# Kernel optimization log

Measured on AMD Instinct MI355X. Metric: run time of the kernel, lower is better.

Reference implementation:

```python
import jax, jax.numpy as jnp
import numpy as np

N = 20000
E = 500000
NS = 128
NT = 128
BN_EPS = 1e-3
DIMS = [NS, 2 * NT, 4 * NT, 2 * NT, NT, NT]


def setup_inputs() -> dict:
    key = jax.random.key(0)
    ks = jax.random.split(key, 32)
    inp = {
        "x": jax.random.normal(ks[0], (N, NS), jnp.float32),
        "edge_index": jax.random.randint(ks[1], (2, E), 0, N),
        "edge_attr": jax.random.uniform(ks[2], (E,), jnp.float32),
    }
    for i in range(5):
        din, dout = DIMS[i], DIMS[i + 1]
        inp[f"W{i+1}"] = jax.random.normal(ks[3 + i], (din, dout), jnp.float32) * (1.0 / np.sqrt(din)).astype(np.float32)
        inp[f"b{i+1}"] = jnp.zeros((dout,), jnp.float32)
    for i in range(4):
        d = DIMS[i + 1]
        inp[f"g{i+1}"] = 1.0 + 0.1 * jax.random.normal(ks[10 + i], (d,), jnp.float32)
        inp[f"be{i+1}"] = 0.1 * jax.random.normal(ks[14 + i], (d,), jnp.float32)
        inp[f"m{i+1}"] = 0.1 * jax.random.normal(ks[18 + i], (d,), jnp.float32)
        inp[f"v{i+1}"] = jax.random.uniform(ks[22 + i], (d,), jnp.float32, minval=0.5, maxval=1.5)
    return inp


def gcn_norm(edge_index, edge_attr, n):
    # PyG gcn_norm with self-loops (fill value 1) and symmetric degree norm.
    loop = jnp.arange(n)
    row = jnp.concatenate([edge_index[0], loop])
    col = jnp.concatenate([edge_index[1], loop])
    w = jnp.concatenate([edge_attr, jnp.ones((n,), edge_attr.dtype)])
    deg = jax.ops.segment_sum(w, col, num_segments=n)
    dinv = jnp.where(deg > 0, jax.lax.rsqrt(deg), 0.0)
    return row, col, dinv[row] * w * dinv[col]


def gcn_conv(h, W, b, row, col, norm, n):
    # out[col] += norm * (h @ W)[row]; then add bias (PyG GCNConv).
    hw = h @ W
    agg = jax.ops.segment_sum(hw[row] * norm[:, None], col, num_segments=n)
    return agg + b


def bn_eval(h, g, be, m, v):
    return (h - m) * jax.lax.rsqrt(v + BN_EPS) * g + be


def reference(x, edge_index, edge_attr,
              W1, b1, W2, b2, W3, b3, W4, b4, W5, b5,
              g1, be1, m1, v1, g2, be2, m2, v2,
              g3, be3, m3, v3, g4, be4, m4, v4):
    n = x.shape[0]
    row, col, norm = gcn_norm(edge_index, edge_attr, n)  # cached=True: shared by all layers
    h = jax.nn.sigmoid(bn_eval(gcn_conv(x, W1, b1, row, col, norm, n), g1, be1, m1, v1))
    h = jax.nn.sigmoid(bn_eval(gcn_conv(h, W2, b2, row, col, norm, n), g2, be2, m2, v2))
    h = jax.nn.sigmoid(bn_eval(gcn_conv(h, W3, b3, row, col, norm, n), g3, be3, m3, v3))
    h = jax.nn.sigmoid(bn_eval(gcn_conv(h, W4, b4, row, col, norm, n), g4, be4, m4, v4))
    h = jax.nn.sigmoid(gcn_conv(h, W5, b5, row, col, norm, n))
    # dropout is identity in eval mode
    x11 = h.T @ h  # [NT, NT]
    x12 = 0.5 * (x11 + x11.T)
    return x12 - jnp.diag(jnp.diag(x12))
```

## Files before the change

### kernel.cpp

```cpp
#include <hip/hip_runtime.h>
#include <hip/hip_bf16.h>
#include <hip/hip_fp8.h>
#include <cstdint>
#include <cstddef>
#include <cstring>

typedef __hip_bfloat16 bf16;
typedef unsigned char fp8;
typedef __attribute__((ext_vector_type(8))) short short8;
typedef __attribute__((ext_vector_type(4))) float f32x4;
typedef __attribute__((ext_vector_type(2))) float f32x2;

#define NSF 128
#define BN_EPS 1e-3f
#define NR 4
#define SCK 2048


__global__ void passA_kernel(const int* __restrict__ ei, int* __restrict__ fill,
                             int* __restrict__ loc, int E, int n, int rsize) {
    int idx = blockIdx.x * blockDim.x + threadIdx.x;
    if (idx < E) {
        int r = ei[idx];
        int c = ei[E + idx];
        int slot = c * NR + r / rsize;
        loc[idx] = atomicAdd(&fill[slot], 1);
    } else if (idx < E + n) {
        int i = idx - E;
        int slot = i * NR + i / rsize;
        loc[idx] = atomicAdd(&fill[slot], 1);
    }
}


__global__ void scan1_kernel(const int* __restrict__ cnt, int* __restrict__ blksum, int total) {
    __shared__ int red[256];
    int base = blockIdx.x * SCK + threadIdx.x * 8;
    int s = 0;
    #pragma unroll
    for (int i = 0; i < 8; ++i) {
        int idx = base + i;
        if (idx < total) s += cnt[idx];
    }
    red[threadIdx.x] = s;
    __syncthreads();
    for (int off2 = 128; off2 > 0; off2 >>= 1) {
        if (threadIdx.x < off2) red[threadIdx.x] += red[threadIdx.x + off2];
        __syncthreads();
    }
    if (threadIdx.x == 0) blksum[blockIdx.x] = red[0];
}

__global__ void scan2_kernel(int* __restrict__ blksum, int* __restrict__ row_ptr,
                             int nblk, int total) {
    __shared__ int part[256];
    int tid = threadIdx.x;
    int v = (tid < nblk) ? blksum[tid] : 0;
    part[tid] = v;
    __syncthreads();
    for (int off2 = 1; off2 < 256; off2 <<= 1) {
        int t = (tid >= off2) ? part[tid - off2] : 0;
        __syncthreads();
        part[tid] += t;
        __syncthreads();
    }
    if (tid < nblk) blksum[tid] = part[tid] - v;
    if (tid == 255) row_ptr[total] = part[255];
}

__global__ void scan3_kernel(const int* __restrict__ cnt, const int* __restrict__ blkoff,
                             int* __restrict__ row_ptr, int total) {
    __shared__ int part[256];
    int tid = threadIdx.x;
    int base = blockIdx.x * SCK + tid * 8;
    int loc[8]; int s = 0;
    #pragma unroll
    for (int i = 0; i < 8; ++i) {
        int idx = base + i;
        loc[i] = (idx < total) ? cnt[idx] : 0;
        s += loc[i];
    }
    part[tid] = s;
    __syncthreads();
    for (int off2 = 1; off2 < 256; off2 <<= 1) {
        int t = (tid >= off2) ? part[tid - off2] : 0;
        __syncthreads();
        part[tid] += t;
        __syncthreads();
    }
    int run = blkoff[blockIdx.x] + part[tid] - s;
    #pragma unroll
    for (int i = 0; i < 8; ++i) {
        int idx = base + i;
        if (idx < total) { row_ptr[idx] = run; run += loc[i]; }
    }
}

__global__ void passB_kernel(const int* __restrict__ ei, const float* __restrict__ ea,
                             const int* __restrict__ row_ptr, const int* __restrict__ loc,
                             int2* __restrict__ e8, int* __restrict__ csr_col,
                             int E, int n, int rsize) {
    int idx = blockIdx.x * blockDim.x + threadIdx.x;
    if (idx < E) {
        int r = ei[idx];
        int c = ei[E + idx];
        int slot = c * NR + r / rsize;
        int p = row_ptr[slot] + loc[idx];
        int2 rec; rec.x = r; rec.y = __float_as_int(ea[idx]);
        e8[p] = rec;
        csr_col[p] = c;
    } else if (idx < E + n) {
        int i = idx - E;
        int slot = i * NR + i / rsize;
        int p = row_ptr[slot] + loc[idx];
        int2 rec; rec.x = i; rec.y = __float_as_int(1.0f);
        e8[p] = rec;
        csr_col[p] = i;
    }
}

__global__ void degdinv_kernel(const int* __restrict__ row_ptr, const int2* __restrict__ e8,
                               float* __restrict__ dinv, int n) {
    int node = blockIdx.x * blockDim.x + threadIdx.x;
    if (node < n) {
        int s = row_ptr[node * NR], e = row_ptr[(node + 1) * NR];
        float d = 0.0f;
        for (int j = s; j < e; ++j) d += __int_as_float(e8[j].y);
        dinv[node] = (d > 0.0f) ? rsqrtf(d) : 0.0f;
    }
}

__global__ void normw_kernel(const float* __restrict__ dinv, const int* __restrict__ csr_col,
                             int2* __restrict__ e8, int EN) {
    int p = blockIdx.x * blockDim.x + threadIdx.x;
    if (p < EN) {
        int2 rec = e8[p];
        float w = dinv[rec.x] * __int_as_float(rec.y) * dinv[csr_col[p]];
        ((int*)e8)[2 * p + 1] = __float_as_int(w);
    }
}


__device__ inline void store_val(bf16* C, size_t idx, float a) {
    C[idx] = __float2bfloat16(a);
}
__device__ inline void store_val(fp8* C, size_t idx, float a) {
    int packed = __builtin_amdgcn_cvt_pk_fp8_f32(a, a, 0, false);
    C[idx] = (fp8)(packed & 0xff);
}

__global__ void prep_kernel(int* __restrict__ fill, int total,
                            const float* __restrict__ x, fp8* __restrict__ xq, int xcnt,
                            const float* __restrict__ W0, const float* __restrict__ W1,
                            const float* __restrict__ W2, const float* __restrict__ W3,
                            const float* __restrict__ W4,
                            bf16* __restrict__ wtbuf, int wtelems) {
    int idx = blockIdx.x * blockDim.x + threadIdx.x;
    if (idx < total) { fill[idx] = 0; return; }
    idx -= total;
    if (idx < xcnt) {
        store_val(xq, idx, x[idx]);
        return;
    }
    int widx = idx - xcnt;
    if (widx >= wtelems) return;
    const float* W; int K, off;
    if (widx < 32768)       { W = W0; K = 128; off = 0; }
    else if (widx < 163840) { W = W1; K = 256; off = 32768; }
    else if (widx < 294912) { W = W2; K = 512; off = 163840; }
    else if (widx < 327680) { W = W3; K = 256; off = 294912; }
    else                    { W = W4; K = 128; off = 327680; }
    int N2;
    if (widx < 32768) N2 = 256; else if (widx < 163840) N2 = 512;
    else if (widx < 294912) N2 = 256; else N2 = 128;
    int l = widx - off;
    int nn = l / K, kk = l % K;
    wtbuf[widx] = __float2bfloat16(W[(size_t)kk * N2 + nn]);
}


__device__ inline void gl_lds16(const bf16* g, bf16* l) {
    __builtin_amdgcn_global_load_lds(
        (const __attribute__((address_space(1))) void*)g,
        (__attribute__((address_space(3))) void*)l,
        16, 0, 0);
}


template <typename OT>
__global__ __launch_bounds__(256) void mfma_gemm_kernel(
    const bf16* __restrict__ A, const bf16* __restrict__ Wt,
    OT* __restrict__ C, int M, int K, int N, int mode,
    const float* __restrict__ bias, const float* __restrict__ g,
    const float* __restrict__ be, const float* __restrict__ m,
    const float* __restrict__ v) {
    __shared__ bf16 As[2][64][32];
    __shared__ bf16 Bs[2][128][32];
    int m0 = blockIdx.x * 64;
    int n0 = blockIdx.y * 128;
    int tid = threadIdx.x;
    int wave = tid >> 6, lane = tid & 63;
    int lrow = lane & 15, quad = lane >> 4;

    f32x4 acc[4][2] = {};

    int srow = lane >> 2;
    int sseg = lane & 3;
    int am = wave * 16 + srow;
    int bn = wave * 32 + srow;
    bool aok = (m0 + am) < M;

    for (int k0 = 0; k0 < K; k0 += 64) {
        if (aok) {
            gl_lds16(A + (size_t)(m0 + am) * K + k0 + sseg * 8,      &As[0][am][sseg * 8]);
            gl_lds16(A + (size_t)(m0 + am) * K + k0 + 32 + sseg * 8, &As[1][am][sseg * 8]);
        }
        gl_lds16(Wt + (size_t)(n0 + bn) * K + k0 + sseg * 8,           &Bs[0][bn][sseg * 8]);
        gl_lds16(Wt + (size_t)(n0 + bn) * K + k0 + 32 + sseg * 8,      &Bs[1][bn][sseg * 8]);
        gl_lds16(Wt + (size_t)(n0 + bn + 16) * K + k0 + sseg * 8,      &Bs[0][bn + 16][sseg * 8]);
        gl_lds16(Wt + (size_t)(n0 + bn + 16) * K + k0 + 32 + sseg * 8, &Bs[1][bn + 16][sseg * 8]);
        __syncthreads();

        #pragma unroll
        for (int ks = 0; ks < 2; ++ks) {
            short8 afrag[4], bfrag[2];
            #pragma unroll
            for (int mt = 0; mt < 4; ++mt)
                afrag[mt] = *(const short8*)(&As[ks][mt * 16 + lrow][quad * 8]);
            #pragma unroll
            for (int nt = 0; nt < 2; ++nt)
                bfrag[nt] = *(const short8*)(&Bs[ks][wave * 32 + nt * 16 + lrow][quad * 8]);
            #pragma unroll
            for (int mt = 0; mt < 4; ++mt)
                #pragma unroll
                for (int nt = 0; nt < 2; ++nt)
                    acc[mt][nt] = __builtin_amdgcn_mfma_f32_16x16x32_bf16(
                        afrag[mt], bfrag[nt], acc[mt][nt], 0, 0, 0);
        }
        __syncthreads();
    }
    #pragma unroll
    for (int nt = 0; nt < 2; ++nt) {
        int gn = n0 + wave * 32 + nt * 16 + lrow;
        float bsc = 0.0f, scale = 1.0f, mean = 0.0f, beta = 0.0f;
        if (mode == 1) {
            bsc = bias[gn];
            scale = g[gn] * rsqrtf(v[gn] + BN_EPS);
            mean = m[gn];
            beta = be[gn];
        }
        #pragma unroll
        for (int mt = 0; mt < 4; ++mt) {
            #pragma unroll
            for (int rr = 0; rr < 4; ++rr) {
                int gm = m0 + mt * 16 + quad * 4 + rr;
                if (gm < M) {
                    float a = acc[mt][nt][rr];
                    if (mode == 1) {
                        a = (a + bsc - mean) * scale + beta;
                        a = 1.0f / (1.0f + __expf(-a));
                    }
                    store_val(C, (size_t)gm * N + gn, a);
                }
            }
        }
    }
}


template <int VEC> struct F8Vec;
template <> struct F8Vec<2> { typedef unsigned short T; };
template <> struct F8Vec<4> { typedef unsigned int T; };

__device__ inline void fma_f8(unsigned short q, float w, float* acc) {
    f32x2 lo = __builtin_amdgcn_cvt_pk_f32_fp8((unsigned int)q, false);
    acc[0] += w * lo.x;
    acc[1] += w * lo.y;
}
__device__ inline void fma_f8(unsigned int q, float w, float* acc) {
    f32x2 lo = __builtin_amdgcn_cvt_pk_f32_fp8(q, false);
    f32x2 hi = __builtin_amdgcn_cvt_pk_f32_fp8(q, true);
    acc[0] += w * lo.x;
    acc[1] += w * lo.y;
    acc[2] += w * hi.x;
    acc[3] += w * hi.y;
}

template <int VEC>
__global__ __launch_bounds__(256) void agg_fp8_kernel(
    const fp8* __restrict__ hw,
    const int* __restrict__ row_ptr, const int2* __restrict__ e8,
    const float* __restrict__ bias,
    const float* __restrict__ g, const float* __restrict__ be,
    const float* __restrict__ m, const float* __restrict__ v,
    bf16* __restrict__ out, int n, int mode) {
    typedef typename F8Vec<VEC>::T T;
    const int dfeat = VEC * 64;
    __shared__ int2 recs[4][64];
    int wave = threadIdx.x >> 6;
    int lane = threadIdx.x & 63;
    int node = blockIdx.x * 4 + wave;
    if (node >= n) return;
    int s = row_ptr[node * NR], e = row_ptr[(node + 1) * NR];
    float acc[VEC];
    #pragma unroll
    for (int i = 0; i < VEC; ++i) acc[i] = 0.0f;
    const unsigned int base = (unsigned int)lane * VEC;

#define LOADG(Q, WV, J0)                                                     \
    _Pragma("unroll")                                                        \
    for (int u = 0; u < 8; ++u) {                                            \
        int2 rec = recs[wave][(J0) + u];                                     \
        WV[u] = __int_as_float(rec.y);                                       \
        Q[u] = *(const T*)(hw + ((unsigned int)rec.x * dfeat + base));       \
    }
#define CONSUME(Q, WV)                                                       \
    _Pragma("unroll")                                                        \
    for (int u = 0; u < 8; ++u) fma_f8(Q[u], WV[u], acc);

    for (int cs = s; cs < e; cs += 64) {
        int cnt = e - cs; if (cnt > 64) cnt = 64;
        int2 r0; r0.x = 0; r0.y = 0;
        if (lane < cnt) r0 = e8[cs + lane];
        recs[wave][lane] = r0;
        asm volatile("s_waitcnt vmcnt(0) lgkmcnt(0)" ::: "memory");

        int npad = (cnt + 15) & ~15;
        T qA[8], qB[8];
        float wA[8], wB[8];
        LOADG(qA, wA, 0)
        LOADG(qB, wB, 8)
        for (int j0 = 16; j0 < npad; j0 += 16) {
            CONSUME(qA, wA)
            LOADG(qA, wA, j0)
            CONSUME(qB, wB)
            LOADG(qB, wB, j0 + 8)
        }
        CONSUME(qA, wA)
        CONSUME(qB, wB)
    }
#undef LOADG
#undef CONSUME

    #pragma unroll
    for (int i = 0; i < VEC; ++i) {
        int f = (int)base + i;
        float a = acc[i];
        if (mode != 0) {
            a += bias[f];
            if (mode == 1) {
                float scale = g[f] * rsqrtf(v[f] + BN_EPS);
                a = (a - m[f]) * scale + be[f];
            }
            a = 1.0f / (1.0f + __expf(-a));
        }
        out[(size_t)node * dfeat + f] = __float2bfloat16(a);
    }
}

#define TPAD 8

__global__ __launch_bounds__(256) void htht_mfma_kernel(
    const bf16* __restrict__ h, float* __restrict__ partial, int n) {
    __shared__ bf16 hsT[128][32 + TPAD];
    int b = blockIdx.x;
    int tid = threadIdx.x;
    int wave = tid >> 6, lane = tid & 63;
    int lrow = lane & 15, quad = lane >> 4;

    f32x4 acc[2][8] = {};

    int kk = tid >> 3;
    int seg = tid & 7;

    for (int kt = 0; kt < 8; ++kt) {
        int k0 = b * 256 + kt * 32;
        #pragma unroll
        for (int s2 = 0; s2 < 2; ++s2) {
            int fs = (seg + s2 * 8) * 8;
            int gk = k0 + kk;
            uint4 q; q.x = q.y = q.z = q.w = 0u;
            if (gk < n) q = *(const uint4*)(h + (size_t)gk * 128 + fs);
            const unsigned short* u = (const unsigned short*)&q;
            #pragma unroll
            for (int i = 0; i < 8; ++i)
                *((unsigned short*)&hsT[fs + i][kk]) = u[i];
        }
        __syncthreads();
        short8 af0 = *(const short8*)(&hsT[wave * 32 + lrow][quad * 8]);
        short8 af1 = *(const short8*)(&hsT[wave * 32 + 16 + lrow][quad * 8]);
        #pragma unroll
        for (int t = 0; t < 8; ++t) {
            short8 bfrag = *(const short8*)(&hsT[t * 16 + lrow][quad * 8]);
            acc[0][t] = __builtin_amdgcn_mfma_f32_16x16x32_bf16(af0, bfrag, acc[0][t], 0, 0, 0);
            acc[1][t] = __builtin_amdgcn_mfma_f32_16x16x32_bf16(af1, bfrag, acc[1][t], 0, 0, 0);
        }
        __syncthreads();
    }
    float* p = partial + (size_t)b * 16384;
    #pragma unroll
    for (int a_ = 0; a_ < 2; ++a_) {
        #pragma unroll
        for (int t = 0; t < 8; ++t) {
            #pragma unroll
            for (int rr = 0; rr < 4; ++rr) {
                int gm = wave * 32 + a_ * 16 + quad * 4 + rr;
                int gn = t * 16 + lrow;
                p[gm * 128 + gn] = acc[a_][t][rr];
            }
        }
    }
}

__global__ void reduce_kernel(const float* __restrict__ partial, float* __restrict__ out, int nchunks) {
    int idx = blockIdx.x * blockDim.x + threadIdx.x;
    float s = 0.0f;
    for (int c = 0; c < nchunks; ++c) s += partial[(size_t)c * 16384 + idx];
    int i = idx / 128, j = idx % 128;
    out[idx] = (i == j) ? 0.0f : s;
}

extern "C" void kernel_launch(void* const* d_in, const int* in_sizes, int n_in,
                              void* d_out, int out_size, void* d_ws, size_t ws_size,
                              hipStream_t stream) {
    const float* x  = (const float*)d_in[0];
    const int*   ei = (const int*)d_in[1];
    const float* ea = (const float*)d_in[2];
    const float* W[5];  const float* bvec[5];
    for (int l = 0; l < 5; ++l) { W[l] = (const float*)d_in[3 + 2 * l]; bvec[l] = (const float*)d_in[4 + 2 * l]; }
    const float* g[4]; const float* be[4]; const float* mm[4]; const float* vv[4];
    for (int l = 0; l < 4; ++l) {
        g[l]  = (const float*)d_in[13 + 4 * l];
        be[l] = (const float*)d_in[14 + 4 * l];
        mm[l] = (const float*)d_in[15 + 4 * l];
        vv[l] = (const float*)d_in[16 + 4 * l];
    }
    const int n = in_sizes[0] / NSF;
    const int E = in_sizes[1] / 2;
    const int EN = E + n;
    const int rsize = (n + NR - 1) / NR;
    const int total = n * NR;
    const int nscan = (total + SCK - 1) / SCK;
    const int dims[6] = {128, 256, 512, 256, 128, 128};
    const int wtoff[5] = {0, 32768, 163840, 294912, 327680};
    const int wtelems = 344064;

    auto align = [](size_t o) { return (o + 255) & ~(size_t)255; };
    size_t off = 0;
    float* dinv    = (float*)((char*)d_ws + off); off = align(off + (size_t)n * 4);
    int*   fill    = (int*)  ((char*)d_ws + off); off = align(off + (size_t)total * 4);
    int*   row_ptr = (int*)  ((char*)d_ws + off); off = align(off + ((size_t)total + 1) * 4);
    int*   blksum  = (int*)  ((char*)d_ws + off); off = align(off + (size_t)256 * 4);
    int*   locb    = (int*)  ((char*)d_ws + off); off = align(off + (size_t)EN * 4);
    int2*  e8      = (int2*) ((char*)d_ws + off); off = align(off + (size_t)EN * 8);
    int*   csr_col = (int*)  ((char*)d_ws + off); off = align(off + (size_t)EN * 4);
    bf16*  wtbuf   = (bf16*) ((char*)d_ws + off); off = align(off + (size_t)wtelems * 2);
    fp8*   xq      = (fp8*)  ((char*)d_ws + off); off = align(off + (size_t)n * 128);
    bf16*  hbuf    = (bf16*) ((char*)d_ws + off); off = align(off + (size_t)n * 512 * 2);
    bf16*  abuf    = (bf16*) ((char*)d_ws + off); off = align(off + (size_t)n * 512 * 2);
    fp8*   f8buf   = (fp8*)  ((char*)d_ws + off); off = align(off + (size_t)n * 256);
    const int KCH = (20000 + 255) / 256;
    float* partial = (float*)((char*)d_ws + off); off = align(off + (size_t)KCH * 16384 * 4);

    {
        int xcnt = n * 128;
        int items = total + xcnt + wtelems;
        prep_kernel<<<(items + 255) / 256, 256, 0, stream>>>(fill, total, x, xq, xcnt,
            W[0], W[1], W[2], W[3], W[4], wtbuf, wtelems);
    }

    passA_kernel<<<(EN + 255) / 256, 256, 0, stream>>>(ei, fill, locb, E, n, rsize);
    scan1_kernel<<<nscan, 256, 0, stream>>>(fill, blksum, total);
    scan2_kernel<<<1, 256, 0, stream>>>(blksum, row_ptr, nscan, total);
    scan3_kernel<<<nscan, 256, 0, stream>>>(fill, blksum, row_ptr, total);
    passB_kernel<<<(EN + 255) / 256, 256, 0, stream>>>(ei, ea, row_ptr, locb,
                                                       e8, csr_col, E, n, rsize);
    degdinv_kernel<<<(n + 255) / 256, 256, 0, stream>>>(row_ptr, e8, dinv, n);
    normw_kernel<<<(EN + 255) / 256, 256, 0, stream>>>(dinv, csr_col, e8, EN);

    int ablocks = (n + 3) / 4;
    auto gemm_bf16 = [&](const bf16* A, int l, bf16* C, int mode) {
        int K = dims[l], N = dims[l + 1];
        dim3 gg((n + 63) / 64, N / 128);
        int bi = (l < 4) ? l : 0;
        mfma_gemm_kernel<bf16><<<gg, 256, 0, stream>>>(A, wtbuf + wtoff[l], C, n, K, N, mode,
                                                       bvec[l], g[bi], be[bi], mm[bi], vv[bi]);
    };
    auto gemm_fp8 = [&](const bf16* A, int l, fp8* C, int mode) {
        int K = dims[l], N = dims[l + 1];
        dim3 gg((n + 63) / 64, N / 128);
        int bi = (l < 4) ? l : 0;
        mfma_gemm_kernel<fp8><<<gg, 256, 0, stream>>>(A, wtbuf + wtoff[l], C, n, K, N, mode,
                                                      bvec[l], g[bi], be[bi], mm[bi], vv[bi]);
    };

    agg_fp8_kernel<2><<<ablocks, 256, 0, stream>>>(xq, row_ptr, e8,
        bvec[0], bvec[0], bvec[0], bvec[0], bvec[0], abuf, n, 0);
    gemm_fp8(abuf, 0, f8buf, 1);
    agg_fp8_kernel<4><<<ablocks, 256, 0, stream>>>(f8buf, row_ptr, e8,
        bvec[1], bvec[1], bvec[1], bvec[1], bvec[1], abuf, n, 0);
    gemm_bf16(abuf, 1, hbuf, 1);
    gemm_fp8(hbuf, 2, f8buf, 0);
    agg_fp8_kernel<4><<<ablocks, 256, 0, stream>>>(f8buf, row_ptr, e8,
        bvec[2], g[2], be[2], mm[2], vv[2], abuf, n, 1);
    gemm_fp8(abuf, 3, f8buf, 0);
    agg_fp8_kernel<2><<<ablocks, 256, 0, stream>>>(f8buf, row_ptr, e8,
        bvec[3], g[3], be[3], mm[3], vv[3], hbuf, n, 1);
    gemm_fp8(hbuf, 4, f8buf, 0);
    agg_fp8_kernel<2><<<ablocks, 256, 0, stream>>>(f8buf, row_ptr, e8,
        bvec[4], bvec[4], bvec[4], bvec[4], bvec[4], abuf, n, 2);

    htht_mfma_kernel<<<KCH, 256, 0, stream>>>(abuf, partial, n);
    reduce_kernel<<<16384 / 256, 256, 0, stream>>>(partial, (float*)d_out, KCH);
}
```

Before: 375.6 us.

## Split 256-wide aggregations by source-node bucket with fp32 atomic accumulation

Replaces the single-pass 256-feature fp8 aggregation with per-bucket passes over the NR source-node buckets of the CSR. The first bucket stores partial sums and the other three atomically add into an fp32 buffer aliased onto hbuf, and a separate epilogue kernel then applies bias, batch-norm and sigmoid. The intent is to shrink the gathered source working set per pass so it fits in cache. In exchange it adds fp32 round trips through global memory, atomics and two extra launches per layer, and it relies on hbuf being large enough to hold the fp32 buffer.

```diff
diff --git a/kernel.cpp b/kernel.cpp
--- a/kernel.cpp
+++ b/kernel.cpp
@@ -286,6 +286,39 @@
     acc[3] += w * hi.y;
 }
 
+#define AGG_GATHER_BODY(SLO, SHI)                                            \
+    for (int cs = (SLO); cs < (SHI); cs += 64) {                             \
+        int cnt = (SHI) - cs; if (cnt > 64) cnt = 64;                        \
+        int2 r0; r0.x = 0; r0.y = 0;                                         \
+        if (lane < cnt) r0 = e8[cs + lane];                                  \
+        recs[wave][lane] = r0;                                               \
+        asm volatile("s_waitcnt vmcnt(0) lgkmcnt(0)" ::: "memory");          \
+        int npad = (cnt + 15) & ~15;                                         \
+        T qA[8], qB[8];                                                      \
+        float wA[8], wB[8];                                                  \
+        LOADG(qA, wA, 0)                                                     \
+        LOADG(qB, wB, 8)                                                     \
+        for (int j0 = 16; j0 < npad; j0 += 16) {                             \
+            CONSUME(qA, wA)                                                  \
+            LOADG(qA, wA, j0)                                                \
+            CONSUME(qB, wB)                                                  \
+            LOADG(qB, wB, j0 + 8)                                            \
+        }                                                                    \
+        CONSUME(qA, wA)                                                      \
+        CONSUME(qB, wB)                                                      \
+    }
+
+#define LOADG(Q, WV, J0)                                                     \
+    _Pragma("unroll")                                                        \
+    for (int u = 0; u < 8; ++u) {                                            \
+        int2 rec = recs[wave][(J0) + u];                                     \
+        WV[u] = __int_as_float(rec.y);                                       \
+        Q[u] = *(const T*)(hw + ((unsigned int)rec.x * dfeat + base));       \
+    }
+#define CONSUME(Q, WV)                                                       \
+    _Pragma("unroll")                                                        \
+    for (int u = 0; u < 8; ++u) fma_f8(Q[u], WV[u], acc);
+
 template <int VEC>
 __global__ __launch_bounds__(256) void agg_fp8_kernel(
     const fp8* __restrict__ hw,
@@ -307,40 +340,7 @@
     for (int i = 0; i < VEC; ++i) acc[i] = 0.0f;
     const unsigned int base = (unsigned int)lane * VEC;
 
-#define LOADG(Q, WV, J0)                                                     \
-    _Pragma("unroll")                                                        \
-    for (int u = 0; u < 8; ++u) {                                            \
-        int2 rec = recs[wave][(J0) + u];                                     \
-        WV[u] = __int_as_float(rec.y);                                       \
-        Q[u] = *(const T*)(hw + ((unsigned int)rec.x * dfeat + base));       \
-    }
-#define CONSUME(Q, WV)                                                       \
-    _Pragma("unroll")                                                        \
-    for (int u = 0; u < 8; ++u) fma_f8(Q[u], WV[u], acc);
-
-    for (int cs = s; cs < e; cs += 64) {
-        int cnt = e - cs; if (cnt > 64) cnt = 64;
-        int2 r0; r0.x = 0; r0.y = 0;
-        if (lane < cnt) r0 = e8[cs + lane];
-        recs[wave][lane] = r0;
-        asm volatile("s_waitcnt vmcnt(0) lgkmcnt(0)" ::: "memory");
-
-        int npad = (cnt + 15) & ~15;
-        T qA[8], qB[8];
-        float wA[8], wB[8];
-        LOADG(qA, wA, 0)
-        LOADG(qB, wB, 8)
-        for (int j0 = 16; j0 < npad; j0 += 16) {
-            CONSUME(qA, wA)
-            LOADG(qA, wA, j0)
-            CONSUME(qB, wB)
-            LOADG(qB, wB, j0 + 8)
-        }
-        CONSUME(qA, wA)
-        CONSUME(qB, wB)
-    }
-#undef LOADG
-#undef CONSUME
+    AGG_GATHER_BODY(s, e)
 
     #pragma unroll
     for (int i = 0; i < VEC; ++i) {
@@ -356,6 +356,65 @@
         }
         out[(size_t)node * dfeat + f] = __float2bfloat16(a);
     }
+}
+
+
+template <int VEC>
+__global__ __launch_bounds__(256) void agg_bucket_kernel(
+    const fp8* __restrict__ hw,
+    const int* __restrict__ row_ptr, const int2* __restrict__ e8,
+    float* __restrict__ accb, int n, int bstart, int store) {
+    typedef typename F8Vec<VEC>::T T;
+    const int dfeat = VEC * 64;
+    __shared__ int2 recs[4][64];
+    int nblk = (n + 3) / 4;
+    int brel = blockIdx.x / nblk;
+    int nb = blockIdx.x - brel * nblk;
+    int bkt = bstart + brel;
+    int wave = threadIdx.x >> 6;
+    int lane = threadIdx.x & 63;
+    int node = nb * 4 + wave;
+    if (node >= n) return;
+    int s = row_ptr[node * NR + bkt], e = row_ptr[node * NR + bkt + 1];
+    float acc[VEC];
+    #pragma unroll
+    for (int i = 0; i < VEC; ++i) acc[i] = 0.0f;
+    const unsigned int base = (unsigned int)lane * VEC;
+
+    AGG_GATHER_BODY(s, e)
+
+    float* ap = accb + (size_t)node * dfeat + base;
+    if (store) {
+        #pragma unroll
+        for (int i = 0; i < VEC; ++i) ap[i] = acc[i];
+    } else {
+        #pragma unroll
+        for (int i = 0; i < VEC; ++i) atomicAdd(&ap[i], acc[i]);
+    }
+}
+
+#undef LOADG
+#undef CONSUME
+#undef AGG_GATHER_BODY
+
+__global__ void agg_epi_kernel(const float* __restrict__ accb,
+                               const float* __restrict__ bias,
+                               const float* __restrict__ g, const float* __restrict__ be,
+                               const float* __restrict__ m, const float* __restrict__ v,
+                               bf16* __restrict__ out, int n, int dfeat, int mode) {
+    int idx = blockIdx.x * blockDim.x + threadIdx.x;
+    if (idx >= n * dfeat) return;
+    int f = idx % dfeat;
+    float a = accb[idx];
+    if (mode != 0) {
+        a += bias[f];
+        if (mode == 1) {
+            float scale = g[f] * rsqrtf(v[f] + BN_EPS);
+            a = (a - m[f]) * scale + be[f];
+        }
+        a = 1.0f / (1.0f + __expf(-a));
+    }
+    out[idx] = __float2bfloat16(a);
 }
 
 #define TPAD 8
@@ -493,16 +552,22 @@
         mfma_gemm_kernel<fp8><<<gg, 256, 0, stream>>>(A, wtbuf + wtoff[l], C, n, K, N, mode,
                                                       bvec[l], g[bi], be[bi], mm[bi], vv[bi]);
     };
+    auto agg4_bucketed = [&](const fp8* in, float* accb, bf16* out,
+                             const float* bias, const float* gg2, const float* bb,
+                             const float* mm2, const float* vv2, int mode) {
+        agg_bucket_kernel<4><<<ablocks, 256, 0, stream>>>(in, row_ptr, e8, accb, n, 0, 1);
+        agg_bucket_kernel<4><<<3 * ablocks, 256, 0, stream>>>(in, row_ptr, e8, accb, n, 1, 0);
+        agg_epi_kernel<<<(n * 256 + 255) / 256, 256, 0, stream>>>(accb, bias, gg2, bb, mm2, vv2,
+                                                                  out, n, 256, mode);
+    };
 
     agg_fp8_kernel<2><<<ablocks, 256, 0, stream>>>(xq, row_ptr, e8,
         bvec[0], bvec[0], bvec[0], bvec[0], bvec[0], abuf, n, 0);
     gemm_fp8(abuf, 0, f8buf, 1);
-    agg_fp8_kernel<4><<<ablocks, 256, 0, stream>>>(f8buf, row_ptr, e8,
-        bvec[1], bvec[1], bvec[1], bvec[1], bvec[1], abuf, n, 0);
+    agg4_bucketed(f8buf, (float*)hbuf, abuf, bvec[1], bvec[1], bvec[1], bvec[1], bvec[1], 0);
     gemm_bf16(abuf, 1, hbuf, 1);
     gemm_fp8(hbuf, 2, f8buf, 0);
-    agg_fp8_kernel<4><<<ablocks, 256, 0, stream>>>(f8buf, row_ptr, e8,
-        bvec[2], g[2], be[2], mm[2], vv[2], abuf, n, 1);
+    agg4_bucketed(f8buf, (float*)hbuf, abuf, bvec[2], g[2], be[2], mm[2], vv[2], 1);
     gemm_fp8(abuf, 3, f8buf, 0);
     agg_fp8_kernel<2><<<ablocks, 256, 0, stream>>>(f8buf, row_ptr, e8,
         bvec[3], g[3], be[3], mm[3], vv[3], hbuf, n, 1);
```

Result: slower. 743.8 us (+98.1%).
